# Kernel tuning notes

Hardware: AMD Instinct MI355X
Metric: run time of the kernel (lower is better)

## Reference

```python
import jax, jax.numpy as jnp
import numpy as np

B, S, H = 1, 2048, 4096
NH = 32
HD = H // NH  # 128
HALF = HD // 2
BASE = 10000.0


def setup_inputs() -> dict:
    key = jax.random.key(0)
    k1, k2, k3 = jax.random.split(key, 3)
    hidden_states = jax.random.normal(k1, (B, S, H), dtype=jnp.float32)
    W_qkv = jax.random.normal(k2, (H, 3 * H), dtype=jnp.float32) * 0.02
    W_o = jax.random.normal(k3, (H, H), dtype=jnp.float32) * 0.02
    # causal additive mask [B,1,S,S]: 0 on/below diagonal, large negative above
    causal = jnp.triu(jnp.full((S, S), -1e9, dtype=jnp.float32), k=1)
    attention_mask = jnp.broadcast_to(causal[None, None], (B, 1, S, S))
    position_ids = jnp.broadcast_to(jnp.arange(S, dtype=jnp.int64)[None, :], (B, S))
    return {
        'hidden_states': hidden_states,
        'W_qkv': W_qkv,
        'W_o': W_o,
        'attention_mask': attention_mask,
        'position_ids': position_ids,
    }


def _rope(x, cos, sin):
    # x: [b,s,nh,hd]; cos/sin: [b,s,1,half]. Half-split rotation as in the Triton kernel.
    x1, x2 = x[..., :HALF], x[..., HALF:]
    return jnp.concatenate([x1 * cos - x2 * sin, x1 * sin + x2 * cos], axis=-1)


def reference(hidden_states, W_qkv, W_o, attention_mask, position_ids):
    b, s, h = hidden_states.shape
    # fused QKV projection (dequantized GPTQ matmul == dense matmul math)
    qkv = jnp.einsum('bsh,hk->bsk', hidden_states, W_qkv).reshape(b, s, 3, NH, HD)
    # RoPE angles: freq = exp(col * INV_BASE) * position_id, INV_BASE = -2 ln(base)/head_dim
    inv_base = -2.0 * np.log(BASE) / HD
    freqs = jnp.exp(jnp.arange(HALF, dtype=jnp.float32) * inv_base)  # [half]
    theta = position_ids.astype(jnp.float32)[:, :, None] * freqs      # [b,s,half]
    cos = jnp.cos(theta)[:, :, None, :]
    sin = jnp.sin(theta)[:, :, None, :]
    q = _rope(qkv[:, :, 0], cos, sin).transpose(0, 2, 1, 3)  # [b,nh,s,hd]
    k = _rope(qkv[:, :, 1], cos, sin).transpose(0, 2, 1, 3)
    v = qkv[:, :, 2].transpose(0, 2, 1, 3)
    scores = jnp.einsum('bhqd,bhkd->bhqk', q, k) / np.sqrt(HD).astype(np.float32)
    scores = scores + attention_mask
    scores = jnp.maximum(scores, jnp.finfo(scores.dtype).min)
    attn = jax.nn.softmax(scores.astype(jnp.float32), axis=-1).astype(q.dtype)
    out = jnp.einsum('bhqk,bhkd->bqhd', attn, v).reshape(b, s, h)
    return jnp.einsum('bsh,ho->bso', out, W_o)
```

## Files before the change

### kernel.cpp

```cpp
#include <hip/hip_runtime.h>

#define S_LEN 2048
#define HDIM 4096
#define NHEADS 32
#define HEAD_DIM 128
#define HALF_DIM 64
#define N_QKV 12288
#define QK_COLS 8192

typedef __attribute__((ext_vector_type(8))) short short8;
typedef __attribute__((ext_vector_type(4))) float f32x4;

typedef const __attribute__((address_space(1))) unsigned int gu32;
typedef __attribute__((address_space(3))) unsigned int lu32;

__device__ __forceinline__ void gload_lds16(const void* g, void* l) {
    __builtin_amdgcn_global_load_lds((gu32*)g, (lu32*)l, 16, 0, 0);
}

__device__ __forceinline__ unsigned short f2bf(float f) {
    unsigned int u = __float_as_uint(f);
    u += 0x7fff + ((u >> 16) & 1);
    return (unsigned short)(u >> 16);
}

__device__ __forceinline__ void xcd_map(int& bx, int& by) {
    int gx = gridDim.x;
    int lin = blockIdx.y * gx + blockIdx.x;
    int x = lin & 7, c = lin >> 3;
    int bxp = gx >> 3;
    bx = bxp * x + c % bxp;
    by = c / bxp;
}


__global__ __launch_bounds__(256) void cvt_hs_k(const float* __restrict__ in,
                                                unsigned short* __restrict__ out, int n4) {
    int i = blockIdx.x * 256 + threadIdx.x;
    if (i >= n4) return;
    float4 v = reinterpret_cast<const float4*>(in)[i];
    ushort4 o;
    o.x = f2bf(v.x); o.y = f2bf(v.y); o.z = f2bf(v.z); o.w = f2bf(v.w);
    reinterpret_cast<ushort4*>(out)[i] = o;
}

__device__ __forceinline__ int permute_col(int n) {
    if (n < QK_COLS) {
        int hd = n & 127;
        int base = n - hd;
        int e = hd & 63;
        int d2 = (e & 15) + 32 * (e >> 4) + ((hd >> 6) << 4);
        return base + d2;
    }
    return n;
}

template <bool PERM>
__global__ __launch_bounds__(256) void tconv_k(const float* __restrict__ in,
                                               unsigned short* __restrict__ out, int R, int C) {
    __shared__ float tile[64][65];
    int c0 = blockIdx.x * 64, r0 = blockIdx.y * 64;
    int tx = threadIdx.x & 63, ty = threadIdx.x >> 6;
#pragma unroll
    for (int i = 0; i < 16; ++i) {
        int r = ty + i * 4;
        tile[r][tx] = in[(size_t)(r0 + r) * C + c0 + tx];
    }
    __syncthreads();
#pragma unroll
    for (int i = 0; i < 16; ++i) {
        int c = ty + i * 4;
        int n = PERM ? permute_col(c0 + c) : (c0 + c);
        out[(size_t)n * R + r0 + tx] = f2bf(tile[tx][c]);
    }
}

__global__ __launch_bounds__(256) void rope_tab_k(const int* __restrict__ pos_raw,
                                                  float* __restrict__ ctab,
                                                  float* __restrict__ stab) {
    int i = blockIdx.x * 256 + threadIdx.x;
    int s = i >> 6, d = i & 63;
    bool is64 = (pos_raw[1] == 0 && pos_raw[2] == 1);
    int p = is64 ? pos_raw[2 * s] : pos_raw[s];
    const float INVB = -0.14391156831212787f;
    float freq = expf((float)d * INVB);
    float th = (float)p * freq;
    ctab[i] = cosf(th);
    stab[i] = sinf(th);
}


__device__ __forceinline__ void mainloop(const unsigned short* __restrict__ Ag,
                                         const unsigned short* __restrict__ Bg,
                                         int K, int m0, int n0,
                                         char* As, char* Bs,
                                         f32x4 (&acc)[4][4]) {
    const int tid = threadIdx.x;
    const int wid = tid >> 6, lane = tid & 63, l15 = lane & 15, l4 = lane >> 4;
    const int wm = wid >> 1, wn = wid & 1;
    const int NT = K >> 6;

    size_t abase[4], bbase[4];
    int off[4];
#pragma unroll
    for (int i = 0; i < 4; ++i) {
        int p = (i * 256 + tid) << 4;
        int q = p ^ (((p >> 7) & 7) << 4);
        abase[i] = (size_t)(m0 + (q >> 7)) * K + ((q & 127) >> 1);
        bbase[i] = (size_t)(n0 + (q >> 7)) * K + ((q & 127) >> 1);
        off[i] = p;
    }

    for (int t = 0; t < NT; ++t) {
        int k0 = t << 6;
#pragma unroll
        for (int i = 0; i < 4; ++i) gload_lds16(Ag + abase[i] + k0, As + off[i]);
#pragma unroll
        for (int i = 0; i < 4; ++i) gload_lds16(Bg + bbase[i] + k0, Bs + off[i]);
        asm volatile("s_waitcnt vmcnt(0)" ::: "memory");
        __builtin_amdgcn_s_barrier();

        short8 a[4][2], b[4][2];
#pragma unroll
        for (int am = 0; am < 4; ++am)
#pragma unroll
            for (int ks = 0; ks < 2; ++ks) {
                int lin = ((wm * 64 + am * 16 + l15) << 7) + ks * 64 + l4 * 16;
                a[am][ks] = *(const short8*)(As + (lin ^ (((lin >> 7) & 7) << 4)));
            }
#pragma unroll
        for (int bn = 0; bn < 4; ++bn)
#pragma unroll
            for (int ks = 0; ks < 2; ++ks) {
                int lin = ((wn * 64 + bn * 16 + l15) << 7) + ks * 64 + l4 * 16;
                b[bn][ks] = *(const short8*)(Bs + (lin ^ (((lin >> 7) & 7) << 4)));
            }
#pragma unroll
        for (int ks = 0; ks < 2; ++ks)
#pragma unroll
            for (int am = 0; am < 4; ++am)
#pragma unroll
                for (int bn = 0; bn < 4; ++bn)
                    acc[am][bn] = __builtin_amdgcn_mfma_f32_16x16x32_bf16(a[am][ks], b[bn][ks], acc[am][bn], 0, 0, 0);

        __builtin_amdgcn_s_barrier();
    }
}

__global__ __launch_bounds__(256, 3) void gemm1_k(const unsigned short* __restrict__ A,
                                                  const unsigned short* __restrict__ Bt,
                                                  const float* __restrict__ ctab,
                                                  const float* __restrict__ stab,
                                                  unsigned short* __restrict__ qb,
                                                  unsigned short* __restrict__ kb,
                                                  unsigned short* __restrict__ vt) {
    __shared__ __attribute__((aligned(16))) char As[16384];
    __shared__ __attribute__((aligned(16))) char Bs[16384];

    int bx, by;
    xcd_map(bx, by);
    int m0 = by * 128, n0 = bx * 128;

    f32x4 acc[4][4];
#pragma unroll
    for (int i = 0; i < 4; ++i)
#pragma unroll
        for (int j = 0; j < 4; ++j) acc[i][j] = (f32x4){0.f, 0.f, 0.f, 0.f};

    mainloop(A, Bt, HDIM, m0, n0, As, Bs, acc);

    int tid = threadIdx.x, wid = tid >> 6, lane = tid & 63, l15 = lane & 15, l4 = lane >> 4;
    int wm = wid >> 1, wn = wid & 1;
    int which = n0 >> 12;
    int head = (n0 & 4095) >> 7;
    if (which < 2) {
        unsigned short* dst = which ? kb : qb;
#pragma unroll
        for (int am = 0; am < 4; ++am)
#pragma unroll
            for (int j = 0; j < 4; ++j) {
                int s = m0 + wm * 64 + am * 16 + l4 * 4 + j;
#pragma unroll
                for (int p = 0; p < 2; ++p) {
                    float x1 = acc[am][2 * p][j], x2 = acc[am][2 * p + 1][j];
                    int e = l15 + 16 * (2 * wn + p);
                    float cs = ctab[s * 64 + e], sn = stab[s * 64 + e];
                    dst[((size_t)head * S_LEN + s) * HEAD_DIM + e] = f2bf(x1 * cs - x2 * sn);
                    dst[((size_t)head * S_LEN + s) * HEAD_DIM + e + 64] = f2bf(x1 * sn + x2 * cs);
                }
            }
    } else {
#pragma unroll
        for (int am = 0; am < 4; ++am)
#pragma unroll
            for (int j = 0; j < 4; ++j) {
                int s = m0 + wm * 64 + am * 16 + l4 * 4 + j;
#pragma unroll
                for (int bn = 0; bn < 4; ++bn) {
                    int d = wn * 64 + bn * 16 + l15;
                    vt[((size_t)head * HEAD_DIM + d) * S_LEN + s] = f2bf(acc[am][bn][j]);
                }
            }
    }
}

__global__ __launch_bounds__(256, 3) void gemm2_k(const unsigned short* __restrict__ A,
                                                  const unsigned short* __restrict__ Bt,
                                                  float* __restrict__ out) {
    __shared__ __attribute__((aligned(16))) char As[16384];
    __shared__ __attribute__((aligned(16))) char Bs[16384];

    int bx, by;
    xcd_map(bx, by);
    int m0 = by * 128, n0 = bx * 128;

    f32x4 acc[4][4];
#pragma unroll
    for (int i = 0; i < 4; ++i)
#pragma unroll
        for (int j = 0; j < 4; ++j) acc[i][j] = (f32x4){0.f, 0.f, 0.f, 0.f};

    mainloop(A, Bt, HDIM, m0, n0, As, Bs, acc);

    int tid = threadIdx.x, wid = tid >> 6, lane = tid & 63, l15 = lane & 15, l4 = lane >> 4;
    int wm = wid >> 1, wn = wid & 1;
#pragma unroll
    for (int am = 0; am < 4; ++am)
#pragma unroll
        for (int j = 0; j < 4; ++j) {
            int s = m0 + wm * 64 + am * 16 + l4 * 4 + j;
#pragma unroll
            for (int bn = 0; bn < 4; ++bn)
                out[(size_t)s * HDIM + n0 + wn * 64 + bn * 16 + l15] = acc[am][bn][j];
        }
}

__global__ __launch_bounds__(256) void flash_k(const unsigned short* __restrict__ Q,
                                               const unsigned short* __restrict__ Kb,
                                               const unsigned short* __restrict__ Vt,
                                               float* __restrict__ O_parts,
                                               float* __restrict__ ml) {
    __shared__ __attribute__((aligned(16))) char Ks[2][16384];
    __shared__ __attribute__((aligned(16))) char Vs[2][16384];
    __shared__ __attribute__((aligned(16))) char Ps[4][4096];
    int h = blockIdx.y;
    int bx2 = 39 - (int)blockIdx.x;
    int qblk, spl;
    if (bx2 < 4)       { qblk = bx2;                 spl = 0; }
    else if (bx2 < 12) { qblk = 4 + ((bx2 - 4) >> 1);  spl = (bx2 - 4) & 1; }
    else if (bx2 < 24) { int u = bx2 - 12; int q3 = u / 3; qblk = 8 + q3; spl = u - 3 * q3; }
    else               { qblk = 12 + ((bx2 - 24) >> 2); spl = (bx2 - 24) & 3; }
    int pidx = h * 40 + bx2;
    int kv_start = spl << 9;
    int kv_end = min((qblk + 1) << 7, (spl + 1) << 9);
    int NT = (kv_end - kv_start) >> 6;

    int tid = threadIdx.x, w = tid >> 6, lane = tid & 63, l15 = lane & 15, l4 = lane >> 4;
    int qrow0 = qblk * 128 + w * 32;

    const unsigned short* Kg = Kb + (size_t)h * S_LEN * HEAD_DIM;
    const unsigned short* Vg = Vt + (size_t)h * HEAD_DIM * S_LEN;

    short8 qf[2][4];
#pragma unroll
    for (int mt = 0; mt < 2; ++mt) {
        int s = qrow0 + mt * 16 + l15;
#pragma unroll
        for (int ks = 0; ks < 4; ++ks)
            qf[mt][ks] = *(const short8*)(Q + ((size_t)h * S_LEN + s) * HEAD_DIM + ks * 32 + l4 * 8);
    }

    float m_run[2][4];
    f32x4 o[2][8];
    f32x4 lsum[2];
#pragma unroll
    for (int mt = 0; mt < 2; ++mt) {
#pragma unroll
        for (int j = 0; j < 4; ++j) m_run[mt][j] = -1e30f;
        lsum[mt] = (f32x4){0.f, 0.f, 0.f, 0.f};
#pragma unroll
        for (int dt = 0; dt < 8; ++dt) o[mt][dt] = (f32x4){0.f, 0.f, 0.f, 0.f};
    }

    int lofs[4];
    size_t kgofs[4], vgofs[4];
#pragma unroll
    for (int i = 0; i < 4; ++i) {
        int p = (i * 256 + tid) << 4;
        lofs[i] = p;
        int qk = p ^ (((p >> 8) & 7) << 4);
        kgofs[i] = (size_t)(qk >> 8) * HEAD_DIM + ((qk & 255) >> 1);
        int qv = p ^ (((p >> 7) & 7) << 4);
        vgofs[i] = (size_t)(qv >> 7) * S_LEN + ((qv & 127) >> 1);
    }

    auto stage = [&](int t) {
        char* Kd = Ks[t & 1];
        char* Vd = Vs[t & 1];
        size_t kvoff = (size_t)(kv_start + t * 64);
#pragma unroll
        for (int i = 0; i < 4; ++i) gload_lds16(Kg + kvoff * HEAD_DIM + kgofs[i], Kd + lofs[i]);
#pragma unroll
        for (int i = 0; i < 4; ++i) gload_lds16(Vg + kvoff + vgofs[i], Vd + lofs[i]);
    };

    const float scale = 0.08838834764831845f;

    short8 onesv;
#pragma unroll
    for (int e = 0; e < 8; ++e) onesv[e] = (short)0x3F80;

    stage(0);

    for (int t = 0; t < NT; ++t) {
        int cur = t & 1;
        if (t + 1 < NT) {
            stage(t + 1);
            asm volatile("s_waitcnt vmcnt(8)" ::: "memory");
        } else {
            asm volatile("s_waitcnt vmcnt(0)" ::: "memory");
        }
        __builtin_amdgcn_sched_barrier(0);
        __builtin_amdgcn_s_barrier();
        __builtin_amdgcn_sched_barrier(0);

        f32x4 sc[2][4];
#pragma unroll
        for (int mt = 0; mt < 2; ++mt)
#pragma unroll
            for (int nt = 0; nt < 4; ++nt) sc[mt][nt] = (f32x4){0.f, 0.f, 0.f, 0.f};
#pragma unroll
        for (int ks = 0; ks < 4; ++ks) {
            short8 kfr[4];
#pragma unroll
            for (int nt = 0; nt < 4; ++nt) {
                int lin = ((nt * 16 + l15) << 8) + ks * 64 + l4 * 16;
                kfr[nt] = *(const short8*)(Ks[cur] + (lin ^ (((lin >> 8) & 7) << 4)));
            }
#pragma unroll
            for (int mt = 0; mt < 2; ++mt)
#pragma unroll
                for (int nt = 0; nt < 4; ++nt)
                    sc[mt][nt] = __builtin_amdgcn_mfma_f32_16x16x32_bf16(qf[mt][ks], kfr[nt], sc[mt][nt], 0, 0, 0);
        }

        float pmax[2][4];
        bool need = false;
#pragma unroll
        for (int mt = 0; mt < 2; ++mt)
#pragma unroll
            for (int j = 0; j < 4; ++j) {
                int srow = qrow0 + mt * 16 + l4 * 4 + j;
                int c = kv_start + t * 64 + l15;
                float v0 = (c      <= srow) ? sc[mt][0][j] * scale : -1e30f;
                float v1 = (c + 16 <= srow) ? sc[mt][1][j] * scale : -1e30f;
                float v2 = (c + 32 <= srow) ? sc[mt][2][j] * scale : -1e30f;
                float v3 = (c + 48 <= srow) ? sc[mt][3][j] * scale : -1e30f;
                sc[mt][0][j] = v0; sc[mt][1][j] = v1; sc[mt][2][j] = v2; sc[mt][3][j] = v3;
                float mx = fmaxf(fmaxf(v0, v1), fmaxf(v2, v3));
                mx = fmaxf(mx, __shfl_xor(mx, 1));
                mx = fmaxf(mx, __shfl_xor(mx, 2));
                mx = fmaxf(mx, __shfl_xor(mx, 4));
                mx = fmaxf(mx, __shfl_xor(mx, 8));
                pmax[mt][j] = mx;
                need = need || (mx > m_run[mt][j] + 8.0f);
            }
        if (__any(need ? 1 : 0)) {
#pragma unroll
            for (int mt = 0; mt < 2; ++mt)
#pragma unroll
                for (int j = 0; j < 4; ++j) {
                    float mnew = fmaxf(m_run[mt][j], pmax[mt][j]);
                    float r = __expf(m_run[mt][j] - mnew);
                    m_run[mt][j] = mnew;
                    lsum[mt][j] *= r;
#pragma unroll
                    for (int dt = 0; dt < 8; ++dt) o[mt][dt][j] *= r;
                }
        }

#pragma unroll
        for (int mt = 0; mt < 2; ++mt)
#pragma unroll
            for (int j = 0; j < 4; ++j) {
                int prow = mt * 16 + l4 * 4 + j;
                int rb = prow << 7;
                int sw = (prow & 7) << 4;
#pragma unroll
                for (int nt = 0; nt < 4; ++nt) {
                    unsigned short pb = f2bf(__expf(sc[mt][nt][j] - m_run[mt][j]));
                    *(unsigned short*)(Ps[w] + ((rb + (l15 + nt * 16) * 2) ^ sw)) = pb;
                }
            }
        asm volatile("s_waitcnt lgkmcnt(0)" ::: "memory");
        __builtin_amdgcn_sched_barrier(0);

        short8 pf[2][2];
#pragma unroll
        for (int mt = 0; mt < 2; ++mt)
#pragma unroll
            for (int k2 = 0; k2 < 2; ++k2) {
                int lin = ((mt * 16 + l15) << 7) + k2 * 64 + l4 * 16;
                pf[mt][k2] = *(const short8*)(Ps[w] + (lin ^ (((lin >> 7) & 7) << 4)));
            }
#pragma unroll
        for (int k2 = 0; k2 < 2; ++k2)
#pragma unroll
            for (int mt = 0; mt < 2; ++mt)
                lsum[mt] = __builtin_amdgcn_mfma_f32_16x16x32_bf16(pf[mt][k2], onesv, lsum[mt], 0, 0, 0);
#pragma unroll
        for (int dt = 0; dt < 8; ++dt) {
#pragma unroll
            for (int k2 = 0; k2 < 2; ++k2) {
                int lin = ((dt * 16 + l15) << 7) + k2 * 64 + l4 * 16;
                short8 vf = *(const short8*)(Vs[cur] + (lin ^ (((lin >> 7) & 7) << 4)));
#pragma unroll
                for (int mt = 0; mt < 2; ++mt)
                    o[mt][dt] = __builtin_amdgcn_mfma_f32_16x16x32_bf16(pf[mt][k2], vf, o[mt][dt], 0, 0, 0);
            }
        }
        __builtin_amdgcn_sched_barrier(0);
        __builtin_amdgcn_s_barrier();
        __builtin_amdgcn_sched_barrier(0);
    }

    float* Op = O_parts + (size_t)pidx * 16384;
#pragma unroll
    for (int mt = 0; mt < 2; ++mt)
#pragma unroll
        for (int j = 0; j < 4; ++j) {
            int rloc = w * 32 + mt * 16 + l4 * 4 + j;
#pragma unroll
            for (int dt = 0; dt < 8; ++dt)
                Op[rloc * 128 + dt * 16 + l15] = o[mt][dt][j];
            if (l15 == 0) {
                ml[(size_t)pidx * 256 + rloc] = m_run[mt][j];
                ml[(size_t)pidx * 256 + 128 + rloc] = lsum[mt][j];
            }
        }
}

__global__ __launch_bounds__(256) void reduce_k(const float* __restrict__ Op,
                                                const float* __restrict__ ml,
                                                unsigned short* __restrict__ ctx) {
    int qblk = blockIdx.x, h = blockIdx.y;
    int ns = (qblk >> 2) + 1;
    int st;
    if (qblk < 4) st = qblk;
    else if (qblk < 8) st = 4 + 2 * (qblk - 4);
    else if (qblk < 12) st = 12 + 3 * (qblk - 8);
    else st = 24 + 4 * (qblk - 12);
    int p0 = h * 40 + st;
#pragma unroll
    for (int it = 0; it < 16; ++it) {
        int idx = it * 256 + threadIdx.x;
        int row = idx >> 5, dq = idx & 31;
        float mstar = -1e30f;
        for (int s = 0; s < ns; ++s)
            mstar = fmaxf(mstar, ml[(size_t)(p0 + s) * 256 + row]);
        f32x4 acc = (f32x4){0.f, 0.f, 0.f, 0.f};
        float lt = 0.f;
        for (int s = 0; s < ns; ++s) {
            float wgt = __expf(ml[(size_t)(p0 + s) * 256 + row] - mstar);
            lt += wgt * ml[(size_t)(p0 + s) * 256 + 128 + row];
            f32x4 ov = *(const f32x4*)(Op + (size_t)(p0 + s) * 16384 + row * 128 + dq * 4);
            acc += ov * wgt;
        }
        float inv = 1.0f / lt;
        int grow = qblk * 128 + row;
        ushort4 o4;
        o4.x = f2bf(acc[0] * inv);
        o4.y = f2bf(acc[1] * inv);
        o4.z = f2bf(acc[2] * inv);
        o4.w = f2bf(acc[3] * inv);
        *(ushort4*)(ctx + (size_t)grow * HDIM + h * 128 + dq * 4) = o4;
    }
}


extern "C" void kernel_launch(void* const* d_in, const int* in_sizes, int n_in,
                              void* d_out, int out_size, void* d_ws, size_t ws_size,
                              hipStream_t stream) {
    const float* hs = (const float*)d_in[0];
    const float* wqkv = (const float*)d_in[1];
    const float* wo = (const float*)d_in[2];
    const int* pos = (const int*)d_in[4];
    float* out = (float*)d_out;
    char* ws = (char*)d_ws;
    const size_t MB = 1024 * 1024;

    unsigned short* hs_b = (unsigned short*)(ws);
    unsigned short* wq_t = (unsigned short*)(ws + 16 * MB);
    unsigned short* wo_t = (unsigned short*)(ws + 112 * MB);
    unsigned short* qbuf = (unsigned short*)(ws + 144 * MB);
    unsigned short* kbuf = (unsigned short*)(ws + 160 * MB);
    unsigned short* vtb  = (unsigned short*)(ws + 176 * MB);
    unsigned short* ctx  = (unsigned short*)(ws + 192 * MB);
    float* ctab = (float*)(ws + 208 * MB);
    float* stab = (float*)(ws + 209 * MB);
    float* O_parts = (float*)(ws + 16 * MB);
    float* ml_buf  = (float*)(ws + 96 * MB);

    cvt_hs_k<<<(S_LEN * HDIM / 4 + 255) / 256, 256, 0, stream>>>(hs, hs_b, S_LEN * HDIM / 4);
    tconv_k<true><<<dim3(N_QKV / 64, HDIM / 64), 256, 0, stream>>>(wqkv, wq_t, HDIM, N_QKV);
    tconv_k<false><<<dim3(HDIM / 64, HDIM / 64), 256, 0, stream>>>(wo, wo_t, HDIM, HDIM);
    rope_tab_k<<<(S_LEN * 64) / 256, 256, 0, stream>>>(pos, ctab, stab);
    gemm1_k<<<dim3(N_QKV / 128, S_LEN / 128), 256, 0, stream>>>(hs_b, wq_t, ctab, stab, qbuf, kbuf, vtb);
    flash_k<<<dim3(40, NHEADS), 256, 0, stream>>>(qbuf, kbuf, vtb, O_parts, ml_buf);
    reduce_k<<<dim3(S_LEN / 128, NHEADS), 256, 0, stream>>>(O_parts, ml_buf, ctx);
    gemm2_k<<<dim3(HDIM / 128, S_LEN / 128), 256, 0, stream>>>(ctx, wo_t, out);
}
```

Measured before the change: 541.1 us.

## Rewrite QKV GEMM with 256x256 tiles, 8 waves, double-buffered LDS ping-pong

The QKV projection kernel moves from 128x128 tiles with 4 waves to 256x256 tiles with 8 waves. LDS loads are double buffered so the next K-slice is fetched while the current one is computed, and the MFMA phases are interleaved with barriers and priority hints. Each block gets more data reuse and global loads overlap with compute. In exchange it uses 128KB of LDS and more registers, and there are fewer blocks (384), which may lower occupancy and hurt wave-quantization balance. The RoPE and V-transpose epilogue is remapped to the new wave layout.

New measurement: 673.4 us. 1.24x slower.

```diff
diff --git a/kernel.cpp b/kernel.cpp
--- a/kernel.cpp
+++ b/kernel.cpp
@@ -147,43 +147,140 @@
     }
 }
 
-__global__ __launch_bounds__(256, 3) void gemm1_k(const unsigned short* __restrict__ A,
+
+#define G1_RDA(SLOT, MBASE)                                                        \
+    _Pragma("unroll")                                                              \
+    for (int mf = 0; mf < 4; ++mf)                                                 \
+        _Pragma("unroll")                                                          \
+        for (int ks = 0; ks < 2; ++ks) {                                           \
+            int lin = ((wm * 128 + (MBASE) + mf * 16 + l15) << 7) + ks * 64 + l4 * 16; \
+            af[mf][ks] = *(const short8*)((SLOT) + (lin ^ (((lin >> 7) & 7) << 4))); \
+        }
+
+#define G1_RDB(SLOT, NBASE, BANK)                                                  \
+    _Pragma("unroll")                                                              \
+    for (int nf = 0; nf < 2; ++nf)                                                 \
+        _Pragma("unroll")                                                          \
+        for (int ks = 0; ks < 2; ++ks) {                                           \
+            int lin = ((wn * 64 + (NBASE) + nf * 16 + l15) << 7) + ks * 64 + l4 * 16; \
+            bf[(BANK) + nf][ks] = *(const short8*)((SLOT) + (lin ^ (((lin >> 7) & 7) << 4))); \
+        }
+
+#define G1_MFMA(MS, NS)                                                            \
+    asm volatile("s_waitcnt lgkmcnt(0)" ::: "memory");                             \
+    __builtin_amdgcn_sched_barrier(0);                                             \
+    __builtin_amdgcn_s_setprio(1);                                                 \
+    _Pragma("unroll")                                                              \
+    for (int ks = 0; ks < 2; ++ks)                                                 \
+        _Pragma("unroll")                                                          \
+        for (int mf = 0; mf < 4; ++mf)                                             \
+            _Pragma("unroll")                                                      \
+            for (int nf = 0; nf < 2; ++nf)                                         \
+                acc[(MS) * 4 + mf][(NS) * 2 + nf] = __builtin_amdgcn_mfma_f32_16x16x32_bf16( \
+                    af[mf][ks], bf[(NS) * 2 + nf][ks], acc[(MS) * 4 + mf][(NS) * 2 + nf], 0, 0, 0); \
+    __builtin_amdgcn_s_setprio(0);
+
+#define G1_BAR() __builtin_amdgcn_s_barrier()
+
+__global__ __launch_bounds__(512, 2) void gemm1_k(const unsigned short* __restrict__ A,
                                                   const unsigned short* __restrict__ Bt,
                                                   const float* __restrict__ ctab,
                                                   const float* __restrict__ stab,
                                                   unsigned short* __restrict__ qb,
                                                   unsigned short* __restrict__ kb,
                                                   unsigned short* __restrict__ vt) {
-    __shared__ __attribute__((aligned(16))) char As[16384];
-    __shared__ __attribute__((aligned(16))) char Bs[16384];
+    __shared__ __attribute__((aligned(16))) char As[2][32768];
+    __shared__ __attribute__((aligned(16))) char Bs[2][32768];
 
     int bx, by;
     xcd_map(bx, by);
-    int m0 = by * 128, n0 = bx * 128;
-
-    f32x4 acc[4][4];
-#pragma unroll
-    for (int i = 0; i < 4; ++i)
+    int m0 = by * 256, n0 = bx * 256;
+
+    const int tid = threadIdx.x;
+    const int wid = tid >> 6, lane = tid & 63, l15 = lane & 15, l4 = lane >> 4;
+    const int wm = wid >> 2, wn = wid & 3;
+
+    int aoff[4], boff[4], asrc[4], bsrc[4];
+#pragma unroll
+    for (int j = 0; j < 4; ++j) {
+        int p = (j * 512 + tid) << 4;
+        int q = p ^ (((p >> 7) & 7) << 4);
+        aoff[j] = p; boff[j] = p;
+        asrc[j] = (m0 + (q >> 7)) * HDIM + ((q & 127) >> 1);
+        bsrc[j] = (n0 + (q >> 7)) * HDIM + ((q & 127) >> 1);
+    }
+
+    auto stage = [&](int t) {
+        char* Ad = As[t & 1];
+        char* Bd = Bs[t & 1];
+        int k0 = t << 6;
+#pragma unroll
+        for (int j = 0; j < 4; ++j) gload_lds16(A + asrc[j] + k0, Ad + aoff[j]);
+#pragma unroll
+        for (int j = 0; j < 4; ++j) gload_lds16(Bt + bsrc[j] + k0, Bd + boff[j]);
+    };
+
+    f32x4 acc[8][4];
+#pragma unroll
+    for (int i = 0; i < 8; ++i)
 #pragma unroll
         for (int j = 0; j < 4; ++j) acc[i][j] = (f32x4){0.f, 0.f, 0.f, 0.f};
 
-    mainloop(A, Bt, HDIM, m0, n0, As, Bs, acc);
-
-    int tid = threadIdx.x, wid = tid >> 6, lane = tid & 63, l15 = lane & 15, l4 = lane >> 4;
-    int wm = wid >> 1, wn = wid & 1;
+    short8 af[4][2], bf[4][2];
+
+    stage(0);
+    for (int i = 0; i < 32; ++i) {
+        char* S0 = As[0]; char* S0b = Bs[0];
+        char* S1 = As[1]; char* S1b = Bs[1];
+        asm volatile("s_waitcnt vmcnt(0)" ::: "memory");
+        G1_BAR();
+        stage(2 * i + 1);
+        G1_RDA(S0, 0) G1_RDB(S0b, 0, 0)
+        G1_BAR();
+        G1_MFMA(0, 0)
+        G1_BAR();
+        G1_RDB(S0b, 32, 2)
+        G1_BAR();
+        G1_MFMA(0, 1)
+        G1_BAR();
+        G1_RDA(S0, 64)
+        G1_BAR();
+        G1_MFMA(1, 0)
+        G1_BAR();
+        G1_BAR();
+        G1_MFMA(1, 1)
+        asm volatile("s_waitcnt vmcnt(0)" ::: "memory");
+        G1_BAR();
+        if (i + 1 < 32) stage(2 * i + 2);
+        G1_RDA(S1, 0) G1_RDB(S1b, 0, 0)
+        G1_BAR();
+        G1_MFMA(0, 0)
+        G1_BAR();
+        G1_RDB(S1b, 32, 2)
+        G1_BAR();
+        G1_MFMA(0, 1)
+        G1_BAR();
+        G1_RDA(S1, 64)
+        G1_BAR();
+        G1_MFMA(1, 0)
+        G1_BAR();
+        G1_BAR();
+        G1_MFMA(1, 1)
+    }
+
     int which = n0 >> 12;
-    int head = (n0 & 4095) >> 7;
     if (which < 2) {
         unsigned short* dst = which ? kb : qb;
-#pragma unroll
-        for (int am = 0; am < 4; ++am)
+        int head = ((n0 & 4095) >> 7) + (wn >> 1);
+#pragma unroll
+        for (int mf = 0; mf < 8; ++mf)
 #pragma unroll
             for (int j = 0; j < 4; ++j) {
-                int s = m0 + wm * 64 + am * 16 + l4 * 4 + j;
-#pragma unroll
-                for (int p = 0; p < 2; ++p) {
-                    float x1 = acc[am][2 * p][j], x2 = acc[am][2 * p + 1][j];
-                    int e = l15 + 16 * (2 * wn + p);
+                int s = m0 + wm * 128 + mf * 16 + l4 * 4 + j;
+#pragma unroll
+                for (int pp = 0; pp < 2; ++pp) {
+                    float x1 = acc[mf][2 * pp][j], x2 = acc[mf][2 * pp + 1][j];
+                    int e = ((wn & 1) * 2 + pp) * 16 + l15;
                     float cs = ctab[s * 64 + e], sn = stab[s * 64 + e];
                     dst[((size_t)head * S_LEN + s) * HEAD_DIM + e] = f2bf(x1 * cs - x2 * sn);
                     dst[((size_t)head * S_LEN + s) * HEAD_DIM + e + 64] = f2bf(x1 * sn + x2 * cs);
@@ -191,14 +288,15 @@
             }
     } else {
 #pragma unroll
-        for (int am = 0; am < 4; ++am)
+        for (int mf = 0; mf < 8; ++mf)
 #pragma unroll
             for (int j = 0; j < 4; ++j) {
-                int s = m0 + wm * 64 + am * 16 + l4 * 4 + j;
-#pragma unroll
-                for (int bn = 0; bn < 4; ++bn) {
-                    int d = wn * 64 + bn * 16 + l15;
-                    vt[((size_t)head * HEAD_DIM + d) * S_LEN + s] = f2bf(acc[am][bn][j]);
+                int s = m0 + wm * 128 + mf * 16 + l4 * 4 + j;
+#pragma unroll
+                for (int nf = 0; nf < 4; ++nf) {
+                    int col = (n0 - QK_COLS) + wn * 64 + nf * 16 + l15;
+                    int head = col >> 7, d = col & 127;
+                    vt[((size_t)head * HEAD_DIM + d) * S_LEN + s] = f2bf(acc[mf][nf][j]);
                 }
             }
     }
@@ -505,7 +603,7 @@
     tconv_k<true><<<dim3(N_QKV / 64, HDIM / 64), 256, 0, stream>>>(wqkv, wq_t, HDIM, N_QKV);
     tconv_k<false><<<dim3(HDIM / 64, HDIM / 64), 256, 0, stream>>>(wo, wo_t, HDIM, HDIM);
     rope_tab_k<<<(S_LEN * 64) / 256, 256, 0, stream>>>(pos, ctab, stab);
-    gemm1_k<<<dim3(N_QKV / 128, S_LEN / 128), 256, 0, stream>>>(hs_b, wq_t, ctab, stab, qbuf, kbuf, vtb);
+    gemm1_k<<<dim3(N_QKV / 256, S_LEN / 256), 512, 0, stream>>>(hs_b, wq_t, ctab, stab, qbuf, kbuf, vtb);
     flash_k<<<dim3(40, NHEADS), 256, 0, stream>>>(qbuf, kbuf, vtb, O_parts, ml_buf);
     reduce_k<<<dim3(S_LEN / 128, NHEADS), 256, 0, stream>>>(O_parts, ml_buf, ctx);
     gemm2_k<<<dim3(HDIM / 128, S_LEN / 128), 256, 0, stream>>>(ctx, wo_t, out);
```
